# Kernel tuning notes

Measured on AMD Instinct MI355X. Metric: run time of the kernel, lower is better.

The kernel has to match this reference:

```python
import jax, jax.numpy as jnp
import numpy as np

TOPK = 32
NUM_PT = 8192
NUM_KP = 8
HW = 19200


def _conv3(x, w, b):
    # x: [1, C, N], w: [O, C, 3] -> [1, O, N] (padding=1)
    y = jax.lax.conv_general_dilated(x, w, (1,), [(1, 1)],
                                     dimension_numbers=('NCH', 'OIH', 'NCH'))
    return y + b[None, :, None]


def setup_inputs() -> dict:
    key = jax.random.key(0)
    ks = jax.random.split(key, 64)

    def p(i, *shape):
        return (jax.random.normal(ks[i], shape, dtype=jnp.float32) * 0.05)

    inp = {
        'seg': jax.random.uniform(ks[0], (1, NUM_PT), dtype=jnp.float32),
        'img': jax.random.normal(ks[1], (1, 32, HW), dtype=jnp.float32),
        'cloud': jax.random.normal(ks[2], (1, NUM_PT, 3), dtype=jnp.float32),
        't': jax.random.normal(ks[3], (1, 3), dtype=jnp.float32),
        'choose': jax.random.randint(ks[4], (1, 1, NUM_PT), 0, HW),
        # Pseudo3DConv params (all 1x1 conv1d == channel matmul)
        'pconv1_w': p(5, 64, 3),    'pconv1_b': p(6, 64),
        'pconv2_w': p(7, 128, 64),  'pconv2_b': p(8, 128),
        'conv1_w': p(9, 64, 32),    'conv1_b': p(10, 64),
        'conv2_w': p(11, 128, 64),  'conv2_b': p(12, 128),
        'psconv1_w': p(13, 256, 128), 'psconv1_b': p(14, 256),
        'psconv2_w': p(15, 128, 256), 'psconv2_b': p(16, 128),
        'final_w': p(17, 128, 416), 'final_b': p(18, 128),
        # heads
        'seg1_w': p(19, 64, 128, 3), 'seg1_b': p(20, 64),
        'seg2_w': p(21, 32, 64),     'seg2_b': p(22, 32),
        'seg3_w': p(23, 1, 32),      'seg3_b': p(24, 1),
        'dis1_w': p(25, 64, 128, 3), 'dis1_b': p(26, 64),
        'dis2_w': p(27, 32, 64),     'dis2_b': p(28, 32),
        'dis3_w': p(29, 1, 32),      'dis3_b': p(30, 1),
        'lin1_w': p(31, 90, 128),    'lin1_b': p(32, 90),
        'lin2_w': p(33, 64, 90),     'lin2_b': p(34, 64),
        'lin3_w': p(35, 3 * NUM_KP, 64), 'lin3_b': p(36, 3 * NUM_KP),
    }
    return inp


def reference(seg, img, cloud, t, choose,
              pconv1_w, pconv1_b, pconv2_w, pconv2_b,
              conv1_w, conv1_b, conv2_w, conv2_b,
              psconv1_w, psconv1_b, psconv2_w, psconv2_b,
              final_w, final_b,
              seg1_w, seg1_b, seg2_w, seg2_b, seg3_w, seg3_b,
              dis1_w, dis1_b, dis2_w, dis2_b, dis3_w, dis3_b,
              lin1_w, lin1_b, lin2_w, lin2_b, lin3_w, lin3_b):
    lrelu = jax.nn.leaky_relu  # slope 0.01, same as torch default
    N = NUM_PT

    # gather per-point image features at chosen pixels: [N, 32]
    feat = jnp.take(img[0], choose[0, 0], axis=1).T
    c = cloud[0]  # [N, 3]

    # ---- KNN (self included, as in knn_cuda) ----
    d2 = jnp.sum((c[:, None, :] - c[None, :, :]) ** 2, axis=-1)  # [N, N]
    _, idx = jax.lax.top_k(-d2, TOPK)  # [N, K] nearest neighbors

    # ---- point-feature MLP (pconv1 -> lrelu -> pconv2) ----
    pf = lrelu(c @ pconv1_w.T + pconv1_b) @ pconv2_w.T + pconv2_b  # [N, 128]

    # ---- vectorized per-point neighbor gather + MLP + weighted maxpool ----
    nf = feat[idx]    # [N, K, 32]
    npf = pf[idx]     # [N, K, 128]
    npos = c[idx]     # [N, K, 3]
    w = jax.nn.softmax(-jnp.linalg.norm(c[:, None, :] - npos, axis=-1), axis=1)  # [N, K]

    f = lrelu(nf @ conv1_w.T + conv1_b) @ conv2_w.T + conv2_b          # [N, K, 128]
    fp = lrelu(npf @ psconv1_w.T + psconv1_b) @ psconv2_w.T + psconv2_b  # [N, K, 128]
    f = jnp.max(f * w[..., None], axis=1)    # [N, 128]
    fp = jnp.max(fp * w[..., None], axis=1)  # [N, 128]

    # final2 = [fp | img_feat], final1 = [f | cloud_feat] -> cat -> [N, 416]
    final = jnp.concatenate([fp, feat, f, pf], axis=1)
    fused = lrelu(final) @ final_w.T + final_b  # [N, 128]
    fused = fused.T[None]  # [1, 128, N]

    def pw(x, w_, b_):  # 1x1 conv1d on [1, C, N]
        return jnp.einsum('oc,bcn->bon', w_, x) + b_[None, :, None]

    # segmentation head
    h = lrelu(_conv3(fused, seg1_w, seg1_b))
    seg_pre = pw(lrelu(pw(h, seg2_w, seg2_b)), seg3_w, seg3_b).reshape(1, N)

    # distance-to-center weighting (norm along coord dim, softmax over points)
    dis_center = jax.nn.softmax(
        jnp.linalg.norm(cloud - (-t)[:, None, :], axis=2), axis=1)  # [1, N]

    # distance head (on unweighted fused features, matching torch op order)
    h = lrelu(_conv3(fused, dis1_w, dis1_b))
    dis_pre = pw(lrelu(pw(h, dis2_w, dis2_b)), dis3_w, dis3_b).reshape(1, N)

    # weight fused features by center distance and segmentation, sum-pool
    fused = fused * dis_center[:, None, :] * seg[:, None, :]
    g = jnp.sum(fused, axis=2)  # [1, 128]

    kp = lrelu(g @ lin1_w.T + lin1_b)
    kp = lrelu(kp @ lin2_w.T + lin2_b)
    keypoints = (kp @ lin3_w.T + lin3_b).reshape(1, NUM_KP, 3)
    return keypoints, dis_pre, dis_center, seg_pre
```

## Files before the change

kernel.cpp:

```cpp
#include <hip/hip_runtime.h>
#include <math.h>

#define NPT 8192
#define HWIMG 19200
#define KCAP 128

using short8 = __attribute__((ext_vector_type(8))) short;
using short4v = __attribute__((ext_vector_type(4))) short;
using f32x4  = __attribute__((ext_vector_type(4))) float;
using f32x2  = __attribute__((ext_vector_type(2))) float;

__device__ __forceinline__ float lrelu(float x) { return x > 0.f ? x : 0.01f * x; }
__device__ __forceinline__ unsigned short f2bf(float v) {
  unsigned u = __float_as_uint(v);
  return (unsigned short)((u + 0x7fffu + ((u >> 16) & 1u)) >> 16);
}
__device__ __forceinline__ float bf2f(unsigned short h) {
  return __uint_as_float(((unsigned)h) << 16);
}
__device__ __forceinline__ void split2(float v, unsigned short& h, unsigned short& l) {
  h = f2bf(v);
  l = f2bf(v - bf2f(h));
}
__device__ __forceinline__ void mfma3(f32x4& acc, short8 ah, short8 al, short8 wh, short8 wl) {
  acc = __builtin_amdgcn_mfma_f32_16x16x32_bf16(ah, wh, acc, 0, 0, 0);
  acc = __builtin_amdgcn_mfma_f32_16x16x32_bf16(al, wh, acc, 0, 0, 0);
  acc = __builtin_amdgcn_mfma_f32_16x16x32_bf16(ah, wl, acc, 0, 0, 0);
}

__device__ __forceinline__ int swz(int o, int k, int Kc) {
  return ((((o >> 4) * Kc + (k >> 5)) << 6) + (((k >> 3) & 3) << 4) + (o & 15)) * 8 + (k & 7);
}

#define OFF_PCONV2  0
#define OFF_CONV1   8192
#define OFF_CONV2   10240
#define OFF_PSCONV1 18432
#define OFF_PSCONV2 51200
#define OFF_FINAL   83968
#define OFF_W3      137216
#define OFF_W2P     186368

#define S_C4    NPT
#define S_G     129
#define S_BIASC 128
#define S_B2C   64
#define S_FEAT  (NPT*32)
#define S_W3    49152
#define S_W2P   8192
#define S_WSPL  OFF_W3
#define PREP_TOTAL (S_C4 + S_G + S_BIASC + S_B2C + S_FEAT + S_W3 + S_W2P + S_WSPL)
__global__ void k_prep(const float* __restrict__ cloud, const int* __restrict__ choose,
                       const float* __restrict__ img,
                       const float* __restrict__ seg1_w, const float* __restrict__ dis1_w,
                       const float* __restrict__ seg1_b, const float* __restrict__ dis1_b,
                       const float* __restrict__ seg2_w, const float* __restrict__ dis2_w,
                       const float* __restrict__ seg2_b, const float* __restrict__ dis2_b,
                       const float* __restrict__ pconv2_w, const float* __restrict__ conv1_w,
                       const float* __restrict__ conv2_w, const float* __restrict__ psconv1_w,
                       const float* __restrict__ psconv2_w, const float* __restrict__ final_w,
                       float* __restrict__ c4, float* __restrict__ soa,
                       float* __restrict__ g,
                       float* __restrict__ biasc, float* __restrict__ bias2c,
                       float* __restrict__ feat,
                       unsigned short* __restrict__ feat_h, unsigned short* __restrict__ feat_l,
                       unsigned short* __restrict__ Wh, unsigned short* __restrict__ Wl) {
  int j = blockIdx.x * blockDim.x + threadIdx.x;
  if (j < S_C4) {
    float x = cloud[j*3+0], y = cloud[j*3+1], z = cloud[j*3+2];
    float4 v; v.x = x; v.y = y; v.z = z; v.w = x*x + y*y + z*z;
    ((float4*)c4)[j] = v;
    soa[j] = x; soa[NPT + j] = y; soa[2*NPT + j] = z; soa[3*NPT + j] = v.w;
    return;
  }
  j -= S_C4;
  if (j < S_G) { g[j] = 0.f; return; }
  j -= S_G;
  if (j < S_BIASC) { biasc[j] = (j < 64) ? seg1_b[j] : dis1_b[j-64]; return; }
  j -= S_BIASC;
  if (j < S_B2C) { bias2c[j] = (j < 32) ? seg2_b[j] : dis2_b[j-32]; return; }
  j -= S_B2C;
  if (j < S_FEAT) {
    int n = j >> 5, ch = j & 31;
    float v = img[ch*HWIMG + choose[n]];
    feat[j] = v;
    unsigned short hh, ll; split2(v, hh, ll);
    int d = swz(n, ch, 1);
    feat_h[d] = hh; feat_l[d] = ll;
    return;
  }
  j -= S_FEAT;
  if (j < S_W3) {
    int h = j / 24576, r = j - h*24576, o = r / 384, k = r - o*384;
    int t = k >> 7, c = k & 127;
    float v = (h ? dis1_w : seg1_w)[o*384 + c*3 + t];
    unsigned short hh, ll; split2(v, hh, ll);
    int d = OFF_W3 + swz(h*64 + o, k, 12);
    Wh[d] = hh; Wl[d] = ll;
    return;
  }
  j -= S_W3;
  if (j < S_W2P) {
    int o = j >> 7, c = j & 127;
    float v = 0.f;
    if (o < 32) { if (c < 64) v = seg2_w[o*64 + c]; }
    else        { if (c >= 64) v = dis2_w[(o-32)*64 + (c-64)]; }
    unsigned short hh, ll; split2(v, hh, ll);
    int d = OFF_W2P + swz(o, c, 4);
    Wh[d] = hh; Wl[d] = ll;
    return;
  }
  j -= S_W2P;
  if (j < S_WSPL) {
    float v; int d;
    if (j < OFF_CONV1) {
      int o = j >> 6, k = j & 63;
      v = pconv2_w[j]; d = OFF_PCONV2 + swz(o, k, 2);
    } else if (j < OFF_CONV2) {
      int jj = j - OFF_CONV1, o = jj >> 5, k = jj & 31;
      v = conv1_w[jj]; d = OFF_CONV1 + swz(o, k, 1);
    } else if (j < OFF_PSCONV1) {
      int jj = j - OFF_CONV2, o = jj >> 6, k = jj & 63;
      v = conv2_w[jj]; d = OFF_CONV2 + swz(o, k, 2);
    } else if (j < OFF_PSCONV2) {
      int jj = j - OFF_PSCONV1, o = jj >> 7, k = jj & 127;
      v = psconv1_w[jj]; d = OFF_PSCONV1 + swz(o, k, 4);
    } else if (j < OFF_FINAL) {
      int jj = j - OFF_PSCONV2, o = jj >> 8, k = jj & 255;
      v = psconv2_w[jj]; d = OFF_PSCONV2 + swz(o, k, 8);
    } else {
      int jj = j - OFF_FINAL, o = jj / 416, k = jj - o*416;
      v = final_w[jj]; d = OFF_FINAL + swz(o, k, 13);
    }
    unsigned short hh, ll; split2(v, hh, ll);
    Wh[d] = hh; Wl[d] = ll;
  }
}

__device__ __forceinline__ unsigned bsort32u(unsigned key, int lane) {
#pragma unroll
  for (int k = 2; k <= 64; k <<= 1) {
#pragma unroll
    for (int j = k >> 1; j > 0; j >>= 1) {
      unsigned o = __shfl_xor(key, j, 64);
      bool keepmin = (((lane & j) == 0) == ((lane & k) == 0));
      key = ((o < key) == keepmin) ? o : key;
    }
  }
  return key;
}
__device__ __forceinline__ unsigned long long bsort64(unsigned long long key, int lane) {
#pragma unroll
  for (int k = 2; k <= 64; k <<= 1) {
#pragma unroll
    for (int j = k >> 1; j > 0; j >>= 1) {
      unsigned long long o = __shfl_xor(key, j, 64);
      bool keepmin = (((lane & j) == 0) == ((lane & k) == 0));
      bool omin = o < key;
      key = (omin == keepmin) ? o : key;
    }
  }
  return key;
}
__device__ __forceinline__ unsigned long long bmerge64(unsigned long long key, int lane) {
#pragma unroll
  for (int j = 32; j > 0; j >>= 1) {
    unsigned long long o = __shfl_xor(key, j, 64);
    bool keepmin = ((lane & j) == 0);
    bool omin = o < key;
    key = (omin == keepmin) ? o : key;
  }
  return key;
}

#define MEGA_GRID 2049
__global__ __launch_bounds__(256) void k_mega(const float4* __restrict__ c4,
                                              const float* __restrict__ soa,
                                              int* __restrict__ idxo, float* __restrict__ wo,
                                              const float* __restrict__ cloud,
                                              const float* __restrict__ tvec,
                                              float* __restrict__ dc,
                                              const float* __restrict__ pconv1_w, const float* __restrict__ pconv1_b,
                                              const float* __restrict__ pconv2_b, const float* __restrict__ psconv1_b,
                                              const float* __restrict__ psconv2_b,
                                              const unsigned short* __restrict__ feat_h,
                                              const unsigned short* __restrict__ feat_l,
                                              const float* __restrict__ conv1_b, const float* __restrict__ conv2_b,
                                              const unsigned short* __restrict__ Wh,
                                              const unsigned short* __restrict__ Wl,
                                              float* __restrict__ pf, float* __restrict__ Yfp,
                                              float* __restrict__ Yf) {
  __shared__ __align__(16) char smem[16384];
  int tid = threadIdx.x, lane = tid & 63, w = tid >> 6;
  int mr = lane & 15, q = lane >> 4;
  if (blockIdx.x > 1024) {
    unsigned short* sh_h = (unsigned short*)smem;
    unsigned short* sh_l = (unsigned short*)(smem + 8192);
    int cb = blockIdx.x - 1025;
    if (cb < 512) {
      int m0 = cb * 16;
      float4 cp = c4[m0 + mr];
      short8 ah0, al0, ah1, al1;
#pragma unroll
      for (int j = 0; j < 8; ++j) {
        int c0 = q*8 + j, c1 = 32 + q*8 + j;
        float v0 = lrelu(fmaf(cp.x, pconv1_w[c0*3+0], fmaf(cp.y, pconv1_w[c0*3+1],
                          fmaf(cp.z, pconv1_w[c0*3+2], pconv1_b[c0]))));
        float v1 = lrelu(fmaf(cp.x, pconv1_w[c1*3+0], fmaf(cp.y, pconv1_w[c1*3+1],
                          fmaf(cp.z, pconv1_w[c1*3+2], pconv1_b[c1]))));
        unsigned short hh, ll;
        split2(v0, hh, ll); ah0[j] = (short)hh; al0[j] = (short)ll;
        split2(v1, hh, ll); ah1[j] = (short)hh; al1[j] = (short)ll;
      }
      f32x4 acc[2];
#pragma unroll
      for (int t = 0; t < 2; ++t) { f32x4 z = {0.f,0.f,0.f,0.f}; acc[t] = z; }
      const unsigned short* W2h = Wh + OFF_PCONV2;
      const unsigned short* W2l = Wl + OFF_PCONV2;
#pragma unroll
      for (int tt = 0; tt < 2; ++tt) {
        int t1 = 2*w + tt;
        int w0 = ((t1*2 + 0)*64 + lane)*8, w1 = ((t1*2 + 1)*64 + lane)*8;
        mfma3(acc[tt], ah0, al0, *(const short8*)(W2h + w0), *(const short8*)(W2l + w0));
        mfma3(acc[tt], ah1, al1, *(const short8*)(W2h + w1), *(const short8*)(W2l + w1));
      }
#pragma unroll
      for (int tt = 0; tt < 2; ++tt) {
        int t1 = 2*w + tt, n = t1*16 + mr;
        float b = pconv2_b[n];
        int ks2 = t1 >> 1, q2 = (t1 & 1)*2 + (mr >> 3), jd = mr & 7;
#pragma unroll
        for (int r = 0; r < 4; ++r) {
          int row = q*4 + r;
          float v = acc[tt][r] + b;
          pf[(size_t)(m0+row)*128 + n] = v;
          unsigned short hh, ll; split2(v, hh, ll);
          int p = ((ks2*16 + row)*4 + q2)*8 + jd;
          sh_h[p] = hh; sh_l[p] = ll;
        }
      }
      __syncthreads();
      f32x4 acc3[2];
#pragma unroll
      for (int t = 0; t < 2; ++t) { f32x4 z = {0.f,0.f,0.f,0.f}; acc3[t] = z; }
      const unsigned short* W3h = Wh + OFF_PSCONV1;
      const unsigned short* W3l = Wl + OFF_PSCONV1;
      const unsigned short* W4h = Wh + OFF_PSCONV2;
      const unsigned short* W4l = Wl + OFF_PSCONV2;
#pragma unroll
      for (int h = 0; h < 2; ++h) {
        f32x4 acc2[2];
#pragma unroll
        for (int t = 0; t < 2; ++t) { f32x4 z = {0.f,0.f,0.f,0.f}; acc2[t] = z; }
#pragma unroll
        for (int ks = 0; ks < 4; ++ks) {
          int ap = ((ks*16 + mr)*4 + q)*8;
          short8 ah = *(const short8*)&sh_h[ap];
          short8 al = *(const short8*)&sh_l[ap];
#pragma unroll
          for (int tt = 0; tt < 2; ++tt) {
            int ts = h*8 + 2*w + tt;
            int wb = ((ts*4 + ks)*64 + lane)*8;
            mfma3(acc2[tt], ah, al, *(const short8*)(W3h + wb), *(const short8*)(W3l + wb));
          }
        }
#pragma unroll
        for (int tt = 0; tt < 2; ++tt) {
          int tl = 2*w + tt;
          int n = h*128 + tl*16 + mr;
          float b = psconv1_b[n];
          int ks3 = tl >> 1, q3 = (tl & 1)*2 + (mr >> 3), jd = mr & 7;
#pragma unroll
          for (int r = 0; r < 4; ++r) {
            int row = q*4 + r;
            float v = lrelu(acc2[tt][r] + b);
            unsigned short hh, ll; split2(v, hh, ll);
            int p = 2048 + ((ks3*16 + row)*4 + q3)*8 + jd;
            sh_h[p] = hh; sh_l[p] = ll;
          }
        }
        __syncthreads();
#pragma unroll
        for (int ks = 0; ks < 4; ++ks) {
          int ap = 2048 + ((ks*16 + mr)*4 + q)*8;
          short8 ah = *(const short8*)&sh_h[ap];
          short8 al = *(const short8*)&sh_l[ap];
#pragma unroll
          for (int tt = 0; tt < 2; ++tt) {
            int wb = (((2*w+tt)*8 + h*4 + ks)*64 + lane)*8;
            mfma3(acc3[tt], ah, al, *(const short8*)(W4h + wb), *(const short8*)(W4l + wb));
          }
        }
        __syncthreads();
      }
#pragma unroll
      for (int tt = 0; tt < 2; ++tt) {
        int n = (2*w+tt)*16 + mr;
        float b = psconv2_b[n];
#pragma unroll
        for (int r = 0; r < 4; ++r)
          Yfp[(size_t)(m0 + q*4 + r)*128 + n] = acc3[tt][r] + b;
      }
    } else {
      int m0 = (cb - 512) * 16;
      int ab = ((m0 >> 4)*64 + lane)*8;
      short8 ah = *(const short8*)(feat_h + ab);
      short8 al = *(const short8*)(feat_l + ab);
      f32x4 acc = {0.f,0.f,0.f,0.f};
      const unsigned short* W1h = Wh + OFF_CONV1;
      const unsigned short* W1l = Wl + OFF_CONV1;
      {
        int wb = (w*64 + lane)*8;
        mfma3(acc, ah, al, *(const short8*)(W1h + wb), *(const short8*)(W1l + wb));
      }
      {
        int n = w*16 + mr;
        float b = conv1_b[n];
        int ks2 = n >> 5, q2 = (n >> 3) & 3, jd = mr & 7;
#pragma unroll
        for (int r = 0; r < 4; ++r) {
          int row = q*4 + r;
          float v = lrelu(acc[r] + b);
          unsigned short hh, ll; split2(v, hh, ll);
          int p = ((ks2*16 + row)*4 + q2)*8 + jd;
          sh_h[p] = hh; sh_l[p] = ll;
        }
      }
      __syncthreads();
      f32x4 acc2[2];
#pragma unroll
      for (int t = 0; t < 2; ++t) { f32x4 z = {0.f,0.f,0.f,0.f}; acc2[t] = z; }
      const unsigned short* W2h = Wh + OFF_CONV2;
      const unsigned short* W2l = Wl + OFF_CONV2;
#pragma unroll
      for (int ks = 0; ks < 2; ++ks) {
        int ap = ((ks*16 + mr)*4 + q)*8;
        short8 a2 = *(const short8*)&sh_h[ap];
        short8 a2l = *(const short8*)&sh_l[ap];
#pragma unroll
        for (int tt = 0; tt < 2; ++tt) {
          int wb = (((2*w+tt)*2 + ks)*64 + lane)*8;
          mfma3(acc2[tt], a2, a2l, *(const short8*)(W2h + wb), *(const short8*)(W2l + wb));
        }
      }
#pragma unroll
      for (int tt = 0; tt < 2; ++tt) {
        int n = (2*w+tt)*16 + mr;
        float b = conv2_b[n];
#pragma unroll
        for (int r = 0; r < 4; ++r)
          Yf[(size_t)(m0 + q*4 + r)*128 + n] = acc2[tt][r] + b;
      }
    }
    return;
  }
  if (blockIdx.x == 1024) {
    float* sred = (float*)smem;
    float tx = tvec[0], ty = tvec[1], tz = tvec[2];
    float v[32];
    float m = -INFINITY;
#pragma unroll
    for (int i2 = 0; i2 < 32; ++i2) {
      int n = i2*256 + tid;
      float ax = cloud[n*3+0] + tx, ay = cloud[n*3+1] + ty, az = cloud[n*3+2] + tz;
      v[i2] = sqrtf(ax*ax + ay*ay + az*az);
      m = fmaxf(m, v[i2]);
    }
#pragma unroll
    for (int o = 1; o < 64; o <<= 1) m = fmaxf(m, __shfl_xor(m, o, 64));
    if (lane == 0) sred[w] = m;
    __syncthreads();
    m = fmaxf(fmaxf(sred[0], sred[1]), fmaxf(sred[2], sred[3]));
    __syncthreads();
    float s = 0.f;
#pragma unroll
    for (int i2 = 0; i2 < 32; ++i2) { v[i2] = expf(v[i2] - m); s += v[i2]; }
#pragma unroll
    for (int o = 1; o < 64; o <<= 1) s += __shfl_xor(s, o, 64);
    if (lane == 0) sred[w] = s;
    __syncthreads();
    s = sred[0] + sred[1] + sred[2] + sred[3];
#pragma unroll
    for (int i2 = 0; i2 < 32; ++i2) dc[i2*256 + tid] = v[i2] / s;
    return;
  }
  float (*smin)[256] = (float(*)[256])smem;
  float (*sd)[KCAP] = (float(*)[KCAP])smem;
  int   (*sj)[KCAP] = (int(*)[KCAP])(smem + 4096);
  float* sTv = (float*)(smem + 8192);
  int*   scnt = (int*)(smem + 8224);
  const float* cx = soa;
  const float* cy = soa + NPT;
  const float* cz = soa + 2*NPT;
  const float* cw = soa + 3*NPT;
  int q0 = blockIdx.x * 8;
  float4 P[8];
#pragma unroll
  for (int i = 0; i < 8; ++i) P[i] = c4[q0 + i];
  f32x2 QX[8], QY[8], QZ[8], QW[8];
#pragma unroll
  for (int i = 0; i < 8; ++i) {
    QX[i][0] = QX[i][1] = -2.f*P[i].x;
    QY[i][0] = QY[i][1] = -2.f*P[i].y;
    QZ[i][0] = QZ[i][1] = -2.f*P[i].z;
    QW[i][0] = QW[i][1] = P[i].w;
  }
#define PDOT(QXI,QYI,QZI,QWI) \
  __builtin_elementwise_fma(X, QXI, __builtin_elementwise_fma(Yv, QYI, \
    __builtin_elementwise_fma(Z, QZI, Wv + QWI)))
  f32x2 inf2 = {INFINITY, INFINITY};
  f32x2 mv[8];
#pragma unroll
  for (int i = 0; i < 8; ++i) mv[i] = inf2;
  for (int t = 0; t < 16; ++t) {
    int j = t*512 + tid*2;
    f32x2 X  = *(const f32x2*)&cx[j];
    f32x2 Yv = *(const f32x2*)&cy[j];
    f32x2 Z  = *(const f32x2*)&cz[j];
    f32x2 Wv = *(const f32x2*)&cw[j];
#pragma unroll
    for (int i = 0; i < 8; ++i)
      mv[i] = __builtin_elementwise_min(mv[i], PDOT(QX[i],QY[i],QZ[i],QW[i]));
  }
#pragma unroll
  for (int i = 0; i < 8; ++i) smin[i][tid] = fminf(mv[i][0], mv[i][1]);
  if (tid < 8) scnt[tid] = 0;
  __syncthreads();
#pragma unroll
  for (int u = 0; u < 2; ++u) {
    int qq = w*2 + u;
    float4 vv = *(const float4*)&smin[qq][lane*4];
    float m4 = fmaxf(fminf(fminf(vv.x, vv.y), fminf(vv.z, vv.w)), 0.f);
    unsigned key = bsort32u(__float_as_uint(m4), lane);
    float T = __uint_as_float(__shfl(key, 31, 64));
    if (lane == 0) sTv[qq] = T * (1.f + 2e-5f) + 4e-5f;
  }
  __syncthreads();
  float Tq[8];
#pragma unroll
  for (int i = 0; i < 8; ++i) Tq[i] = sTv[i];
#define APPEND8(Q, PQ, XX, YY, ZZ, J) { \
    float dx_ = (PQ).x-(XX), dy_ = (PQ).y-(YY), dz_ = (PQ).z-(ZZ); \
    float de_ = dx_*dx_ + dy_*dy_ + dz_*dz_; \
    int p_ = atomicAdd(&scnt[Q],1); if (p_ < KCAP) { sd[Q][p_] = de_; sj[Q][p_] = (J); } }
  for (int t = 0; t < 16; ++t) {
    int j = t*512 + tid*2;
    f32x2 X  = *(const f32x2*)&cx[j];
    f32x2 Yv = *(const f32x2*)&cy[j];
    f32x2 Z  = *(const f32x2*)&cz[j];
    f32x2 Wv = *(const f32x2*)&cw[j];
#pragma unroll
    for (int i = 0; i < 8; ++i) {
      f32x2 d = PDOT(QX[i],QY[i],QZ[i],QW[i]);
      if (d[0] <= Tq[i]) APPEND8(i, P[i], X[0], Yv[0], Z[0], j);
      if (d[1] <= Tq[i]) APPEND8(i, P[i], X[1], Yv[1], Z[1], j+1);
    }
  }
  __syncthreads();
#pragma unroll
  for (int u = 0; u < 2; ++u) {
    int qq = w*2 + u;
    int M = scnt[qq]; if (M > KCAP) M = KCAP;
    unsigned long long key = (lane < M)
        ? (((unsigned long long)__float_as_uint(sd[qq][lane]) << 32) | (unsigned)sj[qq][lane])
        : ~0ull;
    key = bsort64(key, lane);
    for (int base = 64; base < M; base += 64) {
      unsigned long long nk = (base + lane < M)
          ? (((unsigned long long)__float_as_uint(sd[qq][base+lane]) << 32) | (unsigned)sj[qq][base+lane])
          : ~0ull;
      nk = bsort64(nk, lane);
      nk = __shfl_xor(nk, 63, 64);
      key = key < nk ? key : nk;
      key = bmerge64(key, lane);
    }
    float dsel = __uint_as_float((unsigned)(key >> 32));
    int   jsel = (int)(unsigned)(key & 0xffffffffu);
    float v = -sqrtf(dsel);
    float mx = v;
#pragma unroll
    for (int o = 1; o < 32; o <<= 1) mx = fmaxf(mx, __shfl_xor(mx, o, 64));
    float e = expf(v - mx);
    float s = e;
#pragma unroll
    for (int o = 1; o < 32; o <<= 1) s += __shfl_xor(s, o, 64);
    if (lane < 32) {
      int qd = q0 + qq;
      wo[qd*32 + lane] = e / s;
      idxo[qd*32 + lane] = jsel;
    }
  }
}

__global__ __launch_bounds__(512, 4) void k_tail(const float* __restrict__ Yf,
                                              const float* __restrict__ Yfp,
                                              const float* __restrict__ feat,
                                              const float* __restrict__ pf,
                                              const int* __restrict__ idx,
                                              const float* __restrict__ wsm,
                                              const unsigned short* __restrict__ Wh,
                                              const unsigned short* __restrict__ Wl,
                                              const float* __restrict__ final_b,
                                              const float* __restrict__ biasc,
                                              const float* __restrict__ bias2c,
                                              const float* __restrict__ segw, const float* __restrict__ segb,
                                              const float* __restrict__ disw, const float* __restrict__ disb,
                                              const float* __restrict__ dcw, const float* __restrict__ segin,
                                              float* __restrict__ g,
                                              const float* __restrict__ l1w, const float* __restrict__ l1b,
                                              const float* __restrict__ l2w, const float* __restrict__ l2b,
                                              const float* __restrict__ l3w, const float* __restrict__ l3b,
                                              float* __restrict__ osegp, float* __restrict__ odisp,
                                              float* __restrict__ o_kp) {
  __shared__ int sjn[18][32];
  __shared__ float swn[18][32];
  __shared__ int slast;
  __shared__ __align__(16) char sbuf[37440];
  int tid = threadIdx.x, lane = tid & 63, w = tid >> 6;
  int mr = lane & 15, q = lane >> 4;
  int mt = blockIdx.x, m0 = mt * 16;
  for (int t = tid; t < 18*32; t += 512) {
    int lr = t >> 5, k = t & 31, gr = m0 - 1 + lr;
    if (gr >= 0 && gr < NPT) { sjn[lr][k] = idx[gr*32+k]; swn[lr][k] = wsm[gr*32+k]; }
    else { sjn[lr][k] = 0; swn[lr][k] = 0.f; }
  }
  __syncthreads();
  for (int t = tid; t < 1872; t += 512) {
    int lr, col;
    float4 v4;
    if (t < 1152) {
      lr = t >> 6; int arr = (t >> 5) & 1, cg = t & 31;
      const float* Y = arr ? Yf : Yfp;
      float ax = -INFINITY, ay = -INFINITY, az = -INFINITY, aw = -INFINITY;
#pragma unroll
      for (int half = 0; half < 2; ++half) {
        float4 vv[16];
#pragma unroll
        for (int k = 0; k < 16; ++k)
          vv[k] = *(const float4*)&Y[(size_t)sjn[lr][half*16 + k]*128 + cg*4];
#pragma unroll
        for (int k = 0; k < 16; ++k) {
          float wk = swn[lr][half*16 + k];
          ax = fmaxf(ax, wk*vv[k].x); ay = fmaxf(ay, wk*vv[k].y);
          az = fmaxf(az, wk*vv[k].z); aw = fmaxf(aw, wk*vv[k].w);
        }
      }
      v4.x = lrelu(ax); v4.y = lrelu(ay); v4.z = lrelu(az); v4.w = lrelu(aw);
      col = (arr ? 160 : 0) + cg*4;
    } else if (t < 1728) {
      int u = t - 1152; lr = u >> 5; int cg = u & 31;
      int gr = m0 - 1 + lr;
      int gc = gr < 0 ? 0 : (gr >= NPT ? NPT-1 : gr);
      float4 p4 = *(const float4*)&pf[(size_t)gc*128 + cg*4];
      v4.x = lrelu(p4.x); v4.y = lrelu(p4.y); v4.z = lrelu(p4.z); v4.w = lrelu(p4.w);
      col = 288 + cg*4;
    } else {
      int u = t - 1728; lr = u >> 3; int cg = u & 7;
      int gr = m0 - 1 + lr;
      int gc = gr < 0 ? 0 : (gr >= NPT ? NPT-1 : gr);
      float4 p4 = *(const float4*)&feat[(size_t)gc*32 + cg*4];
      v4.x = lrelu(p4.x); v4.y = lrelu(p4.y); v4.z = lrelu(p4.z); v4.w = lrelu(p4.w);
      col = 128 + cg*4;
    }
    int gr = m0 - 1 + lr;
    if (gr < 0 || gr >= NPT) { v4.x = 0.f; v4.y = 0.f; v4.z = 0.f; v4.w = 0.f; }
    int ks = col >> 5, qq = (col >> 3) & 3, j0 = col & 7;
    char* base = sbuf + (ks*18 + lr)*80 + qq*16 + j0*2;
    short4v hv, lv;
    unsigned short hh, ll;
    split2(v4.x, hh, ll); hv[0] = (short)hh; lv[0] = (short)ll;
    split2(v4.y, hh, ll); hv[1] = (short)hh; lv[1] = (short)ll;
    split2(v4.z, hh, ll); hv[2] = (short)hh; lv[2] = (short)ll;
// ... 148 lines not shown
    float a = l1b[tid];
    for (int i = 0; i < 128; ++i) a += sg[i]*l1w[tid*128+i];
    s1[tid] = lrelu(a);
  }
  __syncthreads();
  if (tid < 64) {
    float a = l2b[tid];
    for (int i = 0; i < 90; ++i) a += s1[i]*l2w[tid*90+i];
    s2[tid] = lrelu(a);
  }
  __syncthreads();
  if (tid < 24) {
    float a = l3b[tid];
    for (int i = 0; i < 64; ++i) a += s2[i]*l3w[tid*64+i];
    o_kp[tid] = a;
  }
}

extern "C" void kernel_launch(void* const* d_in, const int* in_sizes, int n_in,
                              void* d_out, int out_size, void* d_ws, size_t ws_size,
                              hipStream_t stream) {
  const float* seg      = (const float*)d_in[0];
  const float* img      = (const float*)d_in[1];
  const float* cloud    = (const float*)d_in[2];
  const float* tvec     = (const float*)d_in[3];
  const int*   choose   = (const int*)d_in[4];
  const float* pconv1_w = (const float*)d_in[5];
  const float* pconv1_b = (const float*)d_in[6];
  const float* pconv2_w = (const float*)d_in[7];
  const float* pconv2_b = (const float*)d_in[8];
  const float* conv1_w  = (const float*)d_in[9];
  const float* conv1_b  = (const float*)d_in[10];
  const float* conv2_w  = (const float*)d_in[11];
  const float* conv2_b  = (const float*)d_in[12];
  const float* psconv1_w= (const float*)d_in[13];
  const float* psconv1_b= (const float*)d_in[14];
  const float* psconv2_w= (const float*)d_in[15];
  const float* psconv2_b= (const float*)d_in[16];
  const float* final_w  = (const float*)d_in[17];
  const float* final_b  = (const float*)d_in[18];
  const float* seg1_w   = (const float*)d_in[19];
  const float* seg1_b   = (const float*)d_in[20];
  const float* seg2_w   = (const float*)d_in[21];
  const float* seg2_b   = (const float*)d_in[22];
  const float* seg3_w   = (const float*)d_in[23];
  const float* seg3_b   = (const float*)d_in[24];
  const float* dis1_w   = (const float*)d_in[25];
  const float* dis1_b   = (const float*)d_in[26];
  const float* dis2_w   = (const float*)d_in[27];
  const float* dis2_b   = (const float*)d_in[28];
  const float* dis3_w   = (const float*)d_in[29];
  const float* dis3_b   = (const float*)d_in[30];
  const float* lin1_w   = (const float*)d_in[31];
  const float* lin1_b   = (const float*)d_in[32];
  const float* lin2_w   = (const float*)d_in[33];
  const float* lin2_b   = (const float*)d_in[34];
  const float* lin3_w   = (const float*)d_in[35];
  const float* lin3_b   = (const float*)d_in[36];

  float* out = (float*)d_out;
  float* ws  = (float*)d_ws;

  float* c4     = ws + 0;
  float* feat   = ws + 32768;
  unsigned short* feat_h = (unsigned short*)(ws + 294912);
  unsigned short* feat_l = (unsigned short*)(ws + 425984);
  float* pf     = ws + 557056;
  float* Yf     = ws + 1605632;
  float* Yfp    = ws + 2654208;
  int*   idx    = (int*)(ws + 3702784);
  float* wsm    = ws + 3964928;
  float* soa    = ws + 4227072;
  unsigned short* Wh    = (unsigned short*)(ws + 9732096);
  unsigned short* Wl    = (unsigned short*)(ws + 9829376);
  float* biasc  = ws + 9926656;
  float* bias2c = ws + 9926784;
  float* g      = ws + 9926848;

  float* o_kp   = out;
  float* o_disp = out + 24;
  float* o_dc   = out + 8216;
  float* o_segp = out + 16408;

  k_prep<<<(PREP_TOTAL + 255)/256, 256, 0, stream>>>(
      cloud, choose, img, seg1_w, dis1_w, seg1_b, dis1_b,
      seg2_w, dis2_w, seg2_b, dis2_b,
      pconv2_w, conv1_w, conv2_w, psconv1_w, psconv2_w, final_w,
      c4, soa, g, biasc, bias2c, feat, feat_h, feat_l, Wh, Wl);

  k_mega<<<MEGA_GRID, 256, 0, stream>>>(
      (const float4*)c4, soa, idx, wsm, cloud, tvec, o_dc,
      pconv1_w, pconv1_b, pconv2_b, psconv1_b, psconv2_b,
      feat_h, feat_l, conv1_b, conv2_b, Wh, Wl, pf, Yfp, Yf);

  k_tail<<<512, 512, 0, stream>>>(
      Yf, Yfp, feat, pf, idx, wsm, Wh, Wl,
      final_b, biasc, bias2c, seg3_w, seg3_b, dis3_w, dis3_b,
      o_dc, seg, g,
      lin1_w, lin1_b, lin2_w, lin2_b, lin3_w, lin3_b,
      o_segp, o_disp, o_kp);

  (void)in_sizes; (void)n_in; (void)out_size; (void)ws_size;
}
```

Before: 225.5 us.

## Move weight/feature prep into the KNN kernel and split the MLP chain into its own kernel

The single prep kernel is split. Cloud and bias setup stay in a small first kernel. Feature gathering and weight bf16 splitting move into extra blocks of the KNN kernel, so they run alongside the KNN search instead of before it. The pointwise MLP chain blocks, which used to share the mega kernel with KNN, become a separate kernel launched afterwards. This adds a launch, and the KNN kernel's shared memory shrinks, which may raise occupancy.

```diff
diff --git a/kernel.cpp b/kernel.cpp
--- a/kernel.cpp
+++ b/kernel.cpp
@@ -41,7 +41,6 @@
 #define OFF_W3      137216
 #define OFF_W2P     186368
 
-#define S_C4    NPT
 #define S_G     129
 #define S_BIASC 128
 #define S_B2C   64
@@ -49,92 +48,29 @@
 #define S_W3    49152
 #define S_W2P   8192
 #define S_WSPL  OFF_W3
-#define PREP_TOTAL (S_C4 + S_G + S_BIASC + S_B2C + S_FEAT + S_W3 + S_W2P + S_WSPL)
-__global__ void k_prep(const float* __restrict__ cloud, const int* __restrict__ choose,
-                       const float* __restrict__ img,
-                       const float* __restrict__ seg1_w, const float* __restrict__ dis1_w,
-                       const float* __restrict__ seg1_b, const float* __restrict__ dis1_b,
-                       const float* __restrict__ seg2_w, const float* __restrict__ dis2_w,
-                       const float* __restrict__ seg2_b, const float* __restrict__ dis2_b,
-                       const float* __restrict__ pconv2_w, const float* __restrict__ conv1_w,
-                       const float* __restrict__ conv2_w, const float* __restrict__ psconv1_w,
-                       const float* __restrict__ psconv2_w, const float* __restrict__ final_w,
-                       float* __restrict__ c4, float* __restrict__ soa,
-                       float* __restrict__ g,
-                       float* __restrict__ biasc, float* __restrict__ bias2c,
-                       float* __restrict__ feat,
-                       unsigned short* __restrict__ feat_h, unsigned short* __restrict__ feat_l,
-                       unsigned short* __restrict__ Wh, unsigned short* __restrict__ Wl) {
+#define PREP_REST (S_FEAT + S_W3 + S_W2P + S_WSPL)
+
+#define P0_TOTAL (NPT + S_G + S_BIASC + S_B2C)
+__global__ void k_prep0(const float* __restrict__ cloud,
+                        const float* __restrict__ seg1_b, const float* __restrict__ dis1_b,
+                        const float* __restrict__ seg2_b, const float* __restrict__ dis2_b,
+                        float* __restrict__ c4, float* __restrict__ soa,
+                        float* __restrict__ g,
+                        float* __restrict__ biasc, float* __restrict__ bias2c) {
   int j = blockIdx.x * blockDim.x + threadIdx.x;
-  if (j < S_C4) {
+  if (j < NPT) {
     float x = cloud[j*3+0], y = cloud[j*3+1], z = cloud[j*3+2];
     float4 v; v.x = x; v.y = y; v.z = z; v.w = x*x + y*y + z*z;
     ((float4*)c4)[j] = v;
     soa[j] = x; soa[NPT + j] = y; soa[2*NPT + j] = z; soa[3*NPT + j] = v.w;
     return;
   }
-  j -= S_C4;
+  j -= NPT;
   if (j < S_G) { g[j] = 0.f; return; }
   j -= S_G;
   if (j < S_BIASC) { biasc[j] = (j < 64) ? seg1_b[j] : dis1_b[j-64]; return; }
   j -= S_BIASC;
-  if (j < S_B2C) { bias2c[j] = (j < 32) ? seg2_b[j] : dis2_b[j-32]; return; }
-  j -= S_B2C;
-  if (j < S_FEAT) {
-    int n = j >> 5, ch = j & 31;
-    float v = img[ch*HWIMG + choose[n]];
-    feat[j] = v;
-    unsigned short hh, ll; split2(v, hh, ll);
-    int d = swz(n, ch, 1);
-    feat_h[d] = hh; feat_l[d] = ll;
-    return;
-  }
-  j -= S_FEAT;
-  if (j < S_W3) {
-    int h = j / 24576, r = j - h*24576, o = r / 384, k = r - o*384;
-    int t = k >> 7, c = k & 127;
-    float v = (h ? dis1_w : seg1_w)[o*384 + c*3 + t];
-    unsigned short hh, ll; split2(v, hh, ll);
-    int d = OFF_W3 + swz(h*64 + o, k, 12);
-    Wh[d] = hh; Wl[d] = ll;
-    return;
-  }
-  j -= S_W3;
-  if (j < S_W2P) {
-    int o = j >> 7, c = j & 127;
-    float v = 0.f;
-    if (o < 32) { if (c < 64) v = seg2_w[o*64 + c]; }
-    else        { if (c >= 64) v = dis2_w[(o-32)*64 + (c-64)]; }
-    unsigned short hh, ll; split2(v, hh, ll);
-    int d = OFF_W2P + swz(o, c, 4);
-    Wh[d] = hh; Wl[d] = ll;
-    return;
-  }
-  j -= S_W2P;
-  if (j < S_WSPL) {
-    float v; int d;
-    if (j < OFF_CONV1) {
-      int o = j >> 6, k = j & 63;
-      v = pconv2_w[j]; d = OFF_PCONV2 + swz(o, k, 2);
-    } else if (j < OFF_CONV2) {
-      int jj = j - OFF_CONV1, o = jj >> 5, k = jj & 31;
-      v = conv1_w[jj]; d = OFF_CONV1 + swz(o, k, 1);
-    } else if (j < OFF_PSCONV1) {
-      int jj = j - OFF_CONV2, o = jj >> 6, k = jj & 63;
-      v = conv2_w[jj]; d = OFF_CONV2 + swz(o, k, 2);
-    } else if (j < OFF_PSCONV2) {
-      int jj = j - OFF_PSCONV1, o = jj >> 7, k = jj & 127;
-      v = psconv1_w[jj]; d = OFF_PSCONV1 + swz(o, k, 4);
-    } else if (j < OFF_FINAL) {
-      int jj = j - OFF_PSCONV2, o = jj >> 8, k = jj & 255;
-      v = psconv2_w[jj]; d = OFF_PSCONV2 + swz(o, k, 8);
-    } else {
-      int jj = j - OFF_FINAL, o = jj / 416, k = jj - o*416;
-      v = final_w[jj]; d = OFF_FINAL + swz(o, k, 13);
-    }
-    unsigned short hh, ll; split2(v, hh, ll);
-    Wh[d] = hh; Wl[d] = ll;
-  }
+  if (j < S_B2C) { bias2c[j] = (j < 32) ? seg2_b[j] : dis2_b[j-32]; }
 }
 
 __device__ __forceinline__ unsigned bsort32u(unsigned key, int lane) {
@@ -173,184 +109,83 @@
   return key;
 }
 
-#define MEGA_GRID 2049
-__global__ __launch_bounds__(256) void k_mega(const float4* __restrict__ c4,
-                                              const float* __restrict__ soa,
-                                              int* __restrict__ idxo, float* __restrict__ wo,
-                                              const float* __restrict__ cloud,
-                                              const float* __restrict__ tvec,
-                                              float* __restrict__ dc,
-                                              const float* __restrict__ pconv1_w, const float* __restrict__ pconv1_b,
-                                              const float* __restrict__ pconv2_b, const float* __restrict__ psconv1_b,
-                                              const float* __restrict__ psconv2_b,
-                                              const unsigned short* __restrict__ feat_h,
-                                              const unsigned short* __restrict__ feat_l,
-                                              const float* __restrict__ conv1_b, const float* __restrict__ conv2_b,
-                                              const unsigned short* __restrict__ Wh,
-                                              const unsigned short* __restrict__ Wl,
-                                              float* __restrict__ pf, float* __restrict__ Yfp,
-                                              float* __restrict__ Yf) {
-  __shared__ __align__(16) char smem[16384];
+#define KP_GRID (1025 + PREP_REST/256)
+__global__ __launch_bounds__(256) void k_knnprep(const float4* __restrict__ c4,
+                                                 const float* __restrict__ soa,
+                                                 int* __restrict__ idxo, float* __restrict__ wo,
+                                                 const float* __restrict__ cloud,
+                                                 const float* __restrict__ tvec,
+                                                 float* __restrict__ dc,
+                                                 const int* __restrict__ choose,
+                                                 const float* __restrict__ img,
+                                                 const float* __restrict__ seg1_w, const float* __restrict__ dis1_w,
+                                                 const float* __restrict__ seg2_w, const float* __restrict__ dis2_w,
+                                                 const float* __restrict__ pconv2_w, const float* __restrict__ conv1_w,
+                                                 const float* __restrict__ conv2_w, const float* __restrict__ psconv1_w,
+                                                 const float* __restrict__ psconv2_w, const float* __restrict__ final_w,
+                                                 float* __restrict__ feat,
+                                                 unsigned short* __restrict__ feat_h,
+                                                 unsigned short* __restrict__ feat_l,
+                                                 unsigned short* __restrict__ Wh,
+                                                 unsigned short* __restrict__ Wl) {
+  __shared__ __align__(16) char smem[8256];
   int tid = threadIdx.x, lane = tid & 63, w = tid >> 6;
-  int mr = lane & 15, q = lane >> 4;
   if (blockIdx.x > 1024) {
-    unsigned short* sh_h = (unsigned short*)smem;
-    unsigned short* sh_l = (unsigned short*)(smem + 8192);
-    int cb = blockIdx.x - 1025;
-    if (cb < 512) {
-      int m0 = cb * 16;
-      float4 cp = c4[m0 + mr];
-      short8 ah0, al0, ah1, al1;
-#pragma unroll
-      for (int j = 0; j < 8; ++j) {
-        int c0 = q*8 + j, c1 = 32 + q*8 + j;
-        float v0 = lrelu(fmaf(cp.x, pconv1_w[c0*3+0], fmaf(cp.y, pconv1_w[c0*3+1],
-                          fmaf(cp.z, pconv1_w[c0*3+2], pconv1_b[c0]))));
-        float v1 = lrelu(fmaf(cp.x, pconv1_w[c1*3+0], fmaf(cp.y, pconv1_w[c1*3+1],
-                          fmaf(cp.z, pconv1_w[c1*3+2], pconv1_b[c1]))));
-        unsigned short hh, ll;
-        split2(v0, hh, ll); ah0[j] = (short)hh; al0[j] = (short)ll;
-        split2(v1, hh, ll); ah1[j] = (short)hh; al1[j] = (short)ll;
+    int j = (blockIdx.x - 1025) * 256 + tid;
+    if (j < S_FEAT) {
+      int n = j >> 5, ch = j & 31;
+      float v = img[ch*HWIMG + choose[n]];
+      feat[j] = v;
+      unsigned short hh, ll; split2(v, hh, ll);
+      int d = swz(n, ch, 1);
+      feat_h[d] = hh; feat_l[d] = ll;
+      return;
+    }
+    j -= S_FEAT;
+    if (j < S_W3) {
+      int h = j / 24576, r = j - h*24576, o = r / 384, k = r - o*384;
+      int t = k >> 7, c = k & 127;
+      float v = (h ? dis1_w : seg1_w)[o*384 + c*3 + t];
+      unsigned short hh, ll; split2(v, hh, ll);
+      int d = OFF_W3 + swz(h*64 + o, k, 12);
+      Wh[d] = hh; Wl[d] = ll;
+      return;
+    }
+    j -= S_W3;
+    if (j < S_W2P) {
+      int o = j >> 7, c = j & 127;
+      float v = 0.f;
+      if (o < 32) { if (c < 64) v = seg2_w[o*64 + c]; }
+      else        { if (c >= 64) v = dis2_w[(o-32)*64 + (c-64)]; }
+      unsigned short hh, ll; split2(v, hh, ll);
+      int d = OFF_W2P + swz(o, c, 4);
+      Wh[d] = hh; Wl[d] = ll;
+      return;
+    }
+    j -= S_W2P;
+    if (j < S_WSPL) {
+      float v; int d;
+      if (j < OFF_CONV1) {
+        int o = j >> 6, k = j & 63;
+        v = pconv2_w[j]; d = OFF_PCONV2 + swz(o, k, 2);
+      } else if (j < OFF_CONV2) {
+        int jj = j - OFF_CONV1, o = jj >> 5, k = jj & 31;
+        v = conv1_w[jj]; d = OFF_CONV1 + swz(o, k, 1);
+      } else if (j < OFF_PSCONV1) {
+        int jj = j - OFF_CONV2, o = jj >> 6, k = jj & 63;
+        v = conv2_w[jj]; d = OFF_CONV2 + swz(o, k, 2);
+      } else if (j < OFF_PSCONV2) {
+        int jj = j - OFF_PSCONV1, o = jj >> 7, k = jj & 127;
+        v = psconv1_w[jj]; d = OFF_PSCONV1 + swz(o, k, 4);
+      } else if (j < OFF_FINAL) {
+        int jj = j - OFF_PSCONV2, o = jj >> 8, k = jj & 255;
+        v = psconv2_w[jj]; d = OFF_PSCONV2 + swz(o, k, 8);
+      } else {
+        int jj = j - OFF_FINAL, o = jj / 416, k = jj - o*416;
+        v = final_w[jj]; d = OFF_FINAL + swz(o, k, 13);
       }
-      f32x4 acc[2];
-#pragma unroll
-      for (int t = 0; t < 2; ++t) { f32x4 z = {0.f,0.f,0.f,0.f}; acc[t] = z; }
-      const unsigned short* W2h = Wh + OFF_PCONV2;
-      const unsigned short* W2l = Wl + OFF_PCONV2;
-#pragma unroll
-      for (int tt = 0; tt < 2; ++tt) {
-        int t1 = 2*w + tt;
-        int w0 = ((t1*2 + 0)*64 + lane)*8, w1 = ((t1*2 + 1)*64 + lane)*8;
-        mfma3(acc[tt], ah0, al0, *(const short8*)(W2h + w0), *(const short8*)(W2l + w0));
-        mfma3(acc[tt], ah1, al1, *(const short8*)(W2h + w1), *(const short8*)(W2l + w1));
-      }
-#pragma unroll
-      for (int tt = 0; tt < 2; ++tt) {
-        int t1 = 2*w + tt, n = t1*16 + mr;
-        float b = pconv2_b[n];
-        int ks2 = t1 >> 1, q2 = (t1 & 1)*2 + (mr >> 3), jd = mr & 7;
-#pragma unroll
-        for (int r = 0; r < 4; ++r) {
-          int row = q*4 + r;
-          float v = acc[tt][r] + b;
-          pf[(size_t)(m0+row)*128 + n] = v;
-          unsigned short hh, ll; split2(v, hh, ll);
-          int p = ((ks2*16 + row)*4 + q2)*8 + jd;
-          sh_h[p] = hh; sh_l[p] = ll;
-        }
-      }
-      __syncthreads();
-      f32x4 acc3[2];
-#pragma unroll
-      for (int t = 0; t < 2; ++t) { f32x4 z = {0.f,0.f,0.f,0.f}; acc3[t] = z; }
-      const unsigned short* W3h = Wh + OFF_PSCONV1;
-      const unsigned short* W3l = Wl + OFF_PSCONV1;
-      const unsigned short* W4h = Wh + OFF_PSCONV2;
-      const unsigned short* W4l = Wl + OFF_PSCONV2;
-#pragma unroll
-      for (int h = 0; h < 2; ++h) {
-        f32x4 acc2[2];
-#pragma unroll
-        for (int t = 0; t < 2; ++t) { f32x4 z = {0.f,0.f,0.f,0.f}; acc2[t] = z; }
-#pragma unroll
-        for (int ks = 0; ks < 4; ++ks) {
-          int ap = ((ks*16 + mr)*4 + q)*8;
-          short8 ah = *(const short8*)&sh_h[ap];
-          short8 al = *(const short8*)&sh_l[ap];
-#pragma unroll
-          for (int tt = 0; tt < 2; ++tt) {
-            int ts = h*8 + 2*w + tt;
-            int wb = ((ts*4 + ks)*64 + lane)*8;
-            mfma3(acc2[tt], ah, al, *(const short8*)(W3h + wb), *(const short8*)(W3l + wb));
-          }
-        }
-#pragma unroll
-        for (int tt = 0; tt < 2; ++tt) {
-          int tl = 2*w + tt;
-          int n = h*128 + tl*16 + mr;
-          float b = psconv1_b[n];
-          int ks3 = tl >> 1, q3 = (tl & 1)*2 + (mr >> 3), jd = mr & 7;
-#pragma unroll
-          for (int r = 0; r < 4; ++r) {
-            int row = q*4 + r;
-            float v = lrelu(acc2[tt][r] + b);
-            unsigned short hh, ll; split2(v, hh, ll);
-            int p = 2048 + ((ks3*16 + row)*4 + q3)*8 + jd;
-            sh_h[p] = hh; sh_l[p] = ll;
-          }
-        }
-        __syncthreads();
-#pragma unroll
-        for (int ks = 0; ks < 4; ++ks) {
-          int ap = 2048 + ((ks*16 + mr)*4 + q)*8;
-          short8 ah = *(const short8*)&sh_h[ap];
-          short8 al = *(const short8*)&sh_l[ap];
-#pragma unroll
-          for (int tt = 0; tt < 2; ++tt) {
-            int wb = (((2*w+tt)*8 + h*4 + ks)*64 + lane)*8;
-            mfma3(acc3[tt], ah, al, *(const short8*)(W4h + wb), *(const short8*)(W4l + wb));
-          }
-        }
-        __syncthreads();
-      }
-#pragma unroll
-      for (int tt = 0; tt < 2; ++tt) {
-        int n = (2*w+tt)*16 + mr;
-        float b = psconv2_b[n];
-#pragma unroll
-        for (int r = 0; r < 4; ++r)
-          Yfp[(size_t)(m0 + q*4 + r)*128 + n] = acc3[tt][r] + b;
-      }
-    } else {
-      int m0 = (cb - 512) * 16;
-      int ab = ((m0 >> 4)*64 + lane)*8;
-      short8 ah = *(const short8*)(feat_h + ab);
-      short8 al = *(const short8*)(feat_l + ab);
-      f32x4 acc = {0.f,0.f,0.f,0.f};
-      const unsigned short* W1h = Wh + OFF_CONV1;
-      const unsigned short* W1l = Wl + OFF_CONV1;
-      {
-        int wb = (w*64 + lane)*8;
-        mfma3(acc, ah, al, *(const short8*)(W1h + wb), *(const short8*)(W1l + wb));
-      }
-      {
-        int n = w*16 + mr;
-        float b = conv1_b[n];
-        int ks2 = n >> 5, q2 = (n >> 3) & 3, jd = mr & 7;
-#pragma unroll
-        for (int r = 0; r < 4; ++r) {
-          int row = q*4 + r;
-          float v = lrelu(acc[r] + b);
-          unsigned short hh, ll; split2(v, hh, ll);
-          int p = ((ks2*16 + row)*4 + q2)*8 + jd;
-          sh_h[p] = hh; sh_l[p] = ll;
-        }
-      }
-      __syncthreads();
-      f32x4 acc2[2];
-#pragma unroll
-      for (int t = 0; t < 2; ++t) { f32x4 z = {0.f,0.f,0.f,0.f}; acc2[t] = z; }
-      const unsigned short* W2h = Wh + OFF_CONV2;
-      const unsigned short* W2l = Wl + OFF_CONV2;
-#pragma unroll
-      for (int ks = 0; ks < 2; ++ks) {
-        int ap = ((ks*16 + mr)*4 + q)*8;
-        short8 a2 = *(const short8*)&sh_h[ap];
-        short8 a2l = *(const short8*)&sh_l[ap];
-#pragma unroll
-        for (int tt = 0; tt < 2; ++tt) {
-          int wb = (((2*w+tt)*2 + ks)*64 + lane)*8;
-          mfma3(acc2[tt], a2, a2l, *(const short8*)(W2h + wb), *(const short8*)(W2l + wb));
-        }
-      }
-#pragma unroll
-      for (int tt = 0; tt < 2; ++tt) {
-        int n = (2*w+tt)*16 + mr;
-        float b = conv2_b[n];
-#pragma unroll
-        for (int r = 0; r < 4; ++r)
-          Yf[(size_t)(m0 + q*4 + r)*128 + n] = acc2[tt][r] + b;
-      }
+      unsigned short hh, ll; split2(v, hh, ll);
+      Wh[d] = hh; Wl[d] = ll;
     }
     return;
   }
@@ -488,6 +323,180 @@
       int qd = q0 + qq;
       wo[qd*32 + lane] = e / s;
       idxo[qd*32 + lane] = jsel;
+    }
+  }
+}
+
+__global__ __launch_bounds__(256) void k_chain(const float4* __restrict__ c4,
+                                               const float* __restrict__ pconv1_w, const float* __restrict__ pconv1_b,
+                                               const float* __restrict__ pconv2_b, const float* __restrict__ psconv1_b,
+                                               const float* __restrict__ psconv2_b,
+                                               const unsigned short* __restrict__ feat_h,
+                                               const unsigned short* __restrict__ feat_l,
+                                               const float* __restrict__ conv1_b, const float* __restrict__ conv2_b,
+                                               const unsigned short* __restrict__ Wh,
+                                               const unsigned short* __restrict__ Wl,
+                                               float* __restrict__ pf, float* __restrict__ Yfp,
+                                               float* __restrict__ Yf) {
+  __shared__ __align__(16) char smem[16384];
+  int tid = threadIdx.x, lane = tid & 63, w = tid >> 6;
+  int mr = lane & 15, q = lane >> 4;
+  unsigned short* sh_h = (unsigned short*)smem;
+  unsigned short* sh_l = (unsigned short*)(smem + 8192);
+  int cb = blockIdx.x;
+  if (cb < 512) {
+    int m0 = cb * 16;
+    float4 cp = c4[m0 + mr];
+    short8 ah0, al0, ah1, al1;
+#pragma unroll
+    for (int j = 0; j < 8; ++j) {
+      int c0 = q*8 + j, c1 = 32 + q*8 + j;
+      float v0 = lrelu(fmaf(cp.x, pconv1_w[c0*3+0], fmaf(cp.y, pconv1_w[c0*3+1],
+                        fmaf(cp.z, pconv1_w[c0*3+2], pconv1_b[c0]))));
+      float v1 = lrelu(fmaf(cp.x, pconv1_w[c1*3+0], fmaf(cp.y, pconv1_w[c1*3+1],
+                        fmaf(cp.z, pconv1_w[c1*3+2], pconv1_b[c1]))));
+      unsigned short hh, ll;
+      split2(v0, hh, ll); ah0[j] = (short)hh; al0[j] = (short)ll;
+      split2(v1, hh, ll); ah1[j] = (short)hh; al1[j] = (short)ll;
+    }
+    f32x4 acc[2];
+#pragma unroll
+    for (int t = 0; t < 2; ++t) { f32x4 z = {0.f,0.f,0.f,0.f}; acc[t] = z; }
+    const unsigned short* W2h = Wh + OFF_PCONV2;
+    const unsigned short* W2l = Wl + OFF_PCONV2;
+#pragma unroll
+    for (int tt = 0; tt < 2; ++tt) {
+      int t1 = 2*w + tt;
+      int w0 = ((t1*2 + 0)*64 + lane)*8, w1 = ((t1*2 + 1)*64 + lane)*8;
+      mfma3(acc[tt], ah0, al0, *(const short8*)(W2h + w0), *(const short8*)(W2l + w0));
+      mfma3(acc[tt], ah1, al1, *(const short8*)(W2h + w1), *(const short8*)(W2l + w1));
+    }
+#pragma unroll
+    for (int tt = 0; tt < 2; ++tt) {
+      int t1 = 2*w + tt, n = t1*16 + mr;
+      float b = pconv2_b[n];
+      int ks2 = t1 >> 1, q2 = (t1 & 1)*2 + (mr >> 3), jd = mr & 7;
+#pragma unroll
+      for (int r = 0; r < 4; ++r) {
+        int row = q*4 + r;
+        float v = acc[tt][r] + b;
+        pf[(size_t)(m0+row)*128 + n] = v;
+        unsigned short hh, ll; split2(v, hh, ll);
+        int p = ((ks2*16 + row)*4 + q2)*8 + jd;
+        sh_h[p] = hh; sh_l[p] = ll;
+      }
+    }
+    __syncthreads();
+    f32x4 acc3[2];
+#pragma unroll
+    for (int t = 0; t < 2; ++t) { f32x4 z = {0.f,0.f,0.f,0.f}; acc3[t] = z; }
+    const unsigned short* W3h = Wh + OFF_PSCONV1;
+    const unsigned short* W3l = Wl + OFF_PSCONV1;
+    const unsigned short* W4h = Wh + OFF_PSCONV2;
+    const unsigned short* W4l = Wl + OFF_PSCONV2;
+#pragma unroll
+    for (int h = 0; h < 2; ++h) {
+      f32x4 acc2[2];
+#pragma unroll
+      for (int t = 0; t < 2; ++t) { f32x4 z = {0.f,0.f,0.f,0.f}; acc2[t] = z; }
+#pragma unroll
+      for (int ks = 0; ks < 4; ++ks) {
+        int ap = ((ks*16 + mr)*4 + q)*8;
+        short8 ah = *(const short8*)&sh_h[ap];
+        short8 al = *(const short8*)&sh_l[ap];
+#pragma unroll
+        for (int tt = 0; tt < 2; ++tt) {
+          int ts = h*8 + 2*w + tt;
+          int wb = ((ts*4 + ks)*64 + lane)*8;
+          mfma3(acc2[tt], ah, al, *(const short8*)(W3h + wb), *(const short8*)(W3l + wb));
+        }
+      }
+#pragma unroll
+      for (int tt = 0; tt < 2; ++tt) {
+        int tl = 2*w + tt;
+        int n = h*128 + tl*16 + mr;
+        float b = psconv1_b[n];
+        int ks3 = tl >> 1, q3 = (tl & 1)*2 + (mr >> 3), jd = mr & 7;
+#pragma unroll
+        for (int r = 0; r < 4; ++r) {
+          int row = q*4 + r;
+          float v = lrelu(acc2[tt][r] + b);
+          unsigned short hh, ll; split2(v, hh, ll);
+          int p = 2048 + ((ks3*16 + row)*4 + q3)*8 + jd;
+          sh_h[p] = hh; sh_l[p] = ll;
+        }
+      }
+      __syncthreads();
+#pragma unroll
+      for (int ks = 0; ks < 4; ++ks) {
+        int ap = 2048 + ((ks*16 + mr)*4 + q)*8;
+        short8 ah = *(const short8*)&sh_h[ap];
+        short8 al = *(const short8*)&sh_l[ap];
+#pragma unroll
+        for (int tt = 0; tt < 2; ++tt) {
+          int wb = (((2*w+tt)*8 + h*4 + ks)*64 + lane)*8;
+          mfma3(acc3[tt], ah, al, *(const short8*)(W4h + wb), *(const short8*)(W4l + wb));
+        }
+      }
+      __syncthreads();
+    }
+#pragma unroll
+    for (int tt = 0; tt < 2; ++tt) {
+      int n = (2*w+tt)*16 + mr;
+      float b = psconv2_b[n];
+#pragma unroll
+      for (int r = 0; r < 4; ++r)
+        Yfp[(size_t)(m0 + q*4 + r)*128 + n] = acc3[tt][r] + b;
+    }
+  } else {
+    int m0 = (cb - 512) * 16;
+    int ab = ((m0 >> 4)*64 + lane)*8;
+    short8 ah = *(const short8*)(feat_h + ab);
+    short8 al = *(const short8*)(feat_l + ab);
+    f32x4 acc = {0.f,0.f,0.f,0.f};
+    const unsigned short* W1h = Wh + OFF_CONV1;
+    const unsigned short* W1l = Wl + OFF_CONV1;
+    {
+      int wb = (w*64 + lane)*8;
+      mfma3(acc, ah, al, *(const short8*)(W1h + wb), *(const short8*)(W1l + wb));
+    }
+    {
+      int n = w*16 + mr;
+      float b = conv1_b[n];
+      int ks2 = n >> 5, q2 = (n >> 3) & 3, jd = mr & 7;
+#pragma unroll
+      for (int r = 0; r < 4; ++r) {
+        int row = q*4 + r;
+        float v = lrelu(acc[r] + b);
+        unsigned short hh, ll; split2(v, hh, ll);
+        int p = ((ks2*16 + row)*4 + q2)*8 + jd;
+        sh_h[p] = hh; sh_l[p] = ll;
+      }
+    }
+    __syncthreads();
+    f32x4 acc2[2];
+#pragma unroll
+    for (int t = 0; t < 2; ++t) { f32x4 z = {0.f,0.f,0.f,0.f}; acc2[t] = z; }
+    const unsigned short* W2h = Wh + OFF_CONV2;
+    const unsigned short* W2l = Wl + OFF_CONV2;
+#pragma unroll
+    for (int ks = 0; ks < 2; ++ks) {
+      int ap = ((ks*16 + mr)*4 + q)*8;
+      short8 a2 = *(const short8*)&sh_h[ap];
+      short8 a2l = *(const short8*)&sh_l[ap];
+#pragma unroll
+      for (int tt = 0; tt < 2; ++tt) {
+        int wb = (((2*w+tt)*2 + ks)*64 + lane)*8;
+        mfma3(acc2[tt], a2, a2l, *(const short8*)(W2h + wb), *(const short8*)(W2l + wb));
+      }
+    }
+#pragma unroll
+    for (int tt = 0; tt < 2; ++tt) {
+      int n = (2*w+tt)*16 + mr;
+      float b = conv2_b[n];
+#pragma unroll
+      for (int r = 0; r < 4; ++r)
+        Yf[(size_t)(m0 + q*4 + r)*128 + n] = acc2[tt][r] + b;
     }
   }
 }
@@ -802,15 +811,18 @@
   float* o_dc   = out + 8216;
   float* o_segp = out + 16408;
 
-  k_prep<<<(PREP_TOTAL + 255)/256, 256, 0, stream>>>(
-      cloud, choose, img, seg1_w, dis1_w, seg1_b, dis1_b,
-      seg2_w, dis2_w, seg2_b, dis2_b,
+  k_prep0<<<(P0_TOTAL + 255)/256, 256, 0, stream>>>(
+      cloud, seg1_b, dis1_b, seg2_b, dis2_b,
+      c4, soa, g, biasc, bias2c);
+
+  k_knnprep<<<KP_GRID, 256, 0, stream>>>(
+      (const float4*)c4, soa, idx, wsm, cloud, tvec, o_dc,
+      choose, img, seg1_w, dis1_w, seg2_w, dis2_w,
       pconv2_w, conv1_w, conv2_w, psconv1_w, psconv2_w, final_w,
-      c4, soa, g, biasc, bias2c, feat, feat_h, feat_l, Wh, Wl);
-
-  k_mega<<<MEGA_GRID, 256, 0, stream>>>(
-      (const float4*)c4, soa, idx, wsm, cloud, tvec, o_dc,
-      pconv1_w, pconv1_b, pconv2_b, psconv1_b, psconv2_b,
+      feat, feat_h, feat_l, Wh, Wl);
+
+  k_chain<<<1024, 256, 0, stream>>>(
+      (const float4*)c4, pconv1_w, pconv1_b, pconv2_b, psconv1_b, psconv2_b,
       feat_h, feat_l, conv1_b, conv2_b, Wh, Wl, pf, Yfp, Yf);
 
   k_tail<<<512, 512, 0, stream>>>(
```

Result: slower. 237.0 us (+5.1%).
